# Kernel tuning notes

Measured on AMD Instinct MI355X. Metric: run time of the kernel, lower is better.

Reference implementation:

```python
import jax, jax.numpy as jnp
import numpy as np

EMB = 1024
HEADS = 16
HEAD_DIM = EMB // HEADS


def setup_inputs() -> dict:
    key = jax.random.key(0)
    ks = jax.random.split(key, 5)
    x = jax.random.normal(ks[0], (2, 2048, EMB), dtype=jnp.float32)
    # per-head projection params, stacked over heads: [H, E, D]
    Wq = jax.random.normal(ks[1], (HEADS, EMB, HEAD_DIM), dtype=jnp.float32)
    Wk = jax.random.normal(ks[2], (HEADS, EMB, HEAD_DIM), dtype=jnp.float32)
    Wv = jax.random.normal(ks[3], (HEADS, EMB, HEAD_DIM), dtype=jnp.float32)
    # output projection (torch Linear weight [out, in], bias=False)
    Wo = jax.random.normal(ks[4], (EMB, EMB), dtype=jnp.float32) * (1.0 / np.sqrt(EMB))
    return {"x": x, "Wq": Wq, "Wk": Wk, "Wv": Wv, "Wo": Wo}


def reference(x, Wq, Wk, Wv, Wo):
    B, T, E = x.shape
    # per-head projections: [B, H, T, D]
    q = jnp.einsum('bte,hed->bhtd', x, Wq)
    k = jnp.einsum('bte,hed->bhtd', x, Wk)
    v = jnp.einsum('bte,hed->bhtd', x, Wv)
    scale = 1.0 / jnp.sqrt(jnp.asarray(HEAD_DIM, dtype=x.dtype))
    scores = jnp.einsum('bhtd,bhsd->bhts', q, k) * scale  # [B,H,T,T]
    s = jax.nn.softmax(scores, axis=-1)
    out = jnp.einsum('bhts,bhsd->bhtd', s, v)
    # concat heads along last dim in head order: [B, T, H*D]
    combined = jnp.transpose(out, (0, 2, 1, 3)).reshape(B, T, E)
    # residual + output projection (Linear bias=False: y = combined @ Wo.T)
    return x + combined @ Wo.T
```

## Files before the change

### kernel.cpp

```cpp
#include <hip/hip_runtime.h>

#define EMB   1024
#define HEADS 16
#define HDIM  64
#define BATCH 2
#define SEQ   2048
#define MROWS (BATCH*SEQ)
#define STR   40
#define QSCALE 0.1803368801111204f

typedef __attribute__((ext_vector_type(8))) short bf16x8;
typedef __attribute__((ext_vector_type(4))) float f32x4;
typedef unsigned short u16;

__device__ __forceinline__ u16 f2bf(float f) {
    unsigned u = __float_as_uint(f);
    u += 0x7fffu + ((u >> 16) & 1u);
    return (u16)(u >> 16);
}
__device__ __forceinline__ float bf2f(u16 h) {
    return __uint_as_float((unsigned)h << 16);
}
__device__ __forceinline__ float fast_exp2(float x) {
#if __has_builtin(__builtin_amdgcn_exp2f)
    return __builtin_amdgcn_exp2f(x);
#else
    return __expf(x * 0.6931471805599453f);
#endif
}
__device__ __forceinline__ unsigned pk_trunc(float lo, float hi) {
    return __builtin_amdgcn_perm(__float_as_uint(hi), __float_as_uint(lo),
                                 0x07060302u);
}

#define SWZ(r, ch) ((((r) << 6)) + ((((ch) ^ ((r) & 7))) << 3))

__global__ __launch_bounds__(256)
void prep1(const float* __restrict__ X, const float* __restrict__ Wq,
           const float* __restrict__ Wk,
           u16* __restrict__ Xh, u16* __restrict__ Xl,
           u16* __restrict__ Qth, u16* __restrict__ Qtl,
           u16* __restrict__ Kth, u16* __restrict__ Ktl)
{
    const int bx = blockIdx.x;
    if (bx < 2048) {
        int i = (bx * 256 + threadIdx.x) * 8;
#pragma unroll
        for (int half = 0; half < 2; ++half) {
            float4 v = *(const float4*)(X + i + half * 4);
            ushort4 hi, lo;
            hi.x = f2bf(v.x); lo.x = f2bf(v.x - bf2f(hi.x));
            hi.y = f2bf(v.y); lo.y = f2bf(v.y - bf2f(hi.y));
            hi.z = f2bf(v.z); lo.z = f2bf(v.z - bf2f(hi.z));
            hi.w = f2bf(v.w); lo.w = f2bf(v.w - bf2f(hi.w));
            *(ushort4*)(Xh + i + half * 4) = hi;
            *(ushort4*)(Xl + i + half * 4) = lo;
        }
    } else {
        const int f = bx - 2048;
        const int z = f >> 9, y = (f >> 5) & 15, x = f & 31;
        const float* W  = z ? Wk  : Wq;
        u16* Oh         = z ? Kth : Qth;
        u16* Ol         = z ? Ktl : Qtl;
        const int d  = threadIdx.x & 63;
        const int e0 = (x * 4 + (threadIdx.x >> 6)) * 8;
        const float* src = W + ((size_t)y * EMB + e0) * HDIM + d;
        ushort4 h0, h1, l0, l1;
        float v; u16 hv;
        v = src[0 * 64]; hv = f2bf(v); h0.x = hv; l0.x = f2bf(v - bf2f(hv));
        v = src[1 * 64]; hv = f2bf(v); h0.y = hv; l0.y = f2bf(v - bf2f(hv));
        v = src[2 * 64]; hv = f2bf(v); h0.z = hv; l0.z = f2bf(v - bf2f(hv));
        v = src[3 * 64]; hv = f2bf(v); h0.w = hv; l0.w = f2bf(v - bf2f(hv));
        v = src[4 * 64]; hv = f2bf(v); h1.x = hv; l1.x = f2bf(v - bf2f(hv));
        v = src[5 * 64]; hv = f2bf(v); h1.y = hv; l1.y = f2bf(v - bf2f(hv));
        v = src[6 * 64]; hv = f2bf(v); h1.z = hv; l1.z = f2bf(v - bf2f(hv));
        v = src[7 * 64]; hv = f2bf(v); h1.w = hv; l1.w = f2bf(v - bf2f(hv));
        size_t obase = ((size_t)y * HDIM + d) * EMB + e0;
        *(ushort4*)(Oh + obase)     = h0;
        *(ushort4*)(Oh + obase + 4) = h1;
        *(ushort4*)(Ol + obase)     = l0;
        *(ushort4*)(Ol + obase + 4) = l1;
    }
}

__global__ __launch_bounds__(256)
void prep2(const float* __restrict__ Wv, const float* __restrict__ Wo,
           u16* __restrict__ Vth, u16* __restrict__ Woh)
{
    const int f = blockIdx.x;
    if (f < 512) {
        const int y = f >> 5, x = f & 31;
        const int d  = threadIdx.x & 63;
        const int e0 = (x * 4 + (threadIdx.x >> 6)) * 8;
        const float* src = Wv + ((size_t)y * EMB + e0) * HDIM + d;
        ushort4 h0, h1;
        h0.x = f2bf(src[0 * 64]); h0.y = f2bf(src[1 * 64]);
        h0.z = f2bf(src[2 * 64]); h0.w = f2bf(src[3 * 64]);
        h1.x = f2bf(src[4 * 64]); h1.y = f2bf(src[5 * 64]);
        h1.z = f2bf(src[6 * 64]); h1.w = f2bf(src[7 * 64]);
        size_t obase = ((size_t)y * HDIM + d) * EMB + e0;
        *(ushort4*)(Vth + obase)     = h0;
        *(ushort4*)(Vth + obase + 4) = h1;
    } else {
        int i = ((f - 512) * 256 + threadIdx.x) * 8;
#pragma unroll
        for (int half = 0; half < 2; ++half) {
            float4 v = *(const float4*)(Wo + i + half * 4);
            ushort4 o;
            o.x = f2bf(v.x); o.y = f2bf(v.y); o.z = f2bf(v.z); o.w = f2bf(v.w);
            *(ushort4*)(Woh + i + half * 4) = o;
        }
    }
}

__global__ __launch_bounds__(256, 2)
void qkv_z01(const u16* __restrict__ Xh, const u16* __restrict__ Xl,
             const u16* __restrict__ Wqh, const u16* __restrict__ Wql,
             const u16* __restrict__ Wkh, const u16* __restrict__ Wkl,
             u16* __restrict__ Qh, u16* __restrict__ Ql,
             u16* __restrict__ Kh, u16* __restrict__ Kl)
{
    const int z  = blockIdx.z;
    const int m0 = blockIdx.x * 128;
    const int n0 = blockIdx.y * 128;
    const int t    = threadIdx.x;
    const int wave = t >> 6, lane = t & 63;
    const int wm = wave & 1, wn = wave >> 1;
    const int l16 = lane & 15, quad = lane >> 4;

    __shared__ u16 Ahs[128][STR];
    __shared__ u16 Als[128][STR];
    __shared__ u16 Bhs[128][STR];
    __shared__ u16 Bls[128][STR];

    const u16* Bh_g = z ? Wkh : Wqh;
    const u16* Bl_g = z ? Wkl : Wql;

    const int ar0 = t >> 2, ak = (t & 3) * 8, ar1 = ar0 + 64;

    f32x4 acc[4][4];
#pragma unroll
    for (int i = 0; i < 4; ++i)
#pragma unroll
        for (int j = 0; j < 4; ++j) acc[i][j] = (f32x4){0.f, 0.f, 0.f, 0.f};

    bf16x8 cur[8], nxt[8], nx2[8];
#define QK_LOAD(dst, kk)                                                        \
    do {                                                                        \
        dst[0] = *(const bf16x8*)(Xh  + (size_t)(m0 + ar0) * EMB + (kk) + ak);  \
        dst[1] = *(const bf16x8*)(Xh  + (size_t)(m0 + ar1) * EMB + (kk) + ak);  \
        dst[2] = *(const bf16x8*)(Xl  + (size_t)(m0 + ar0) * EMB + (kk) + ak);  \
        dst[3] = *(const bf16x8*)(Xl  + (size_t)(m0 + ar1) * EMB + (kk) + ak);  \
        dst[4] = *(const bf16x8*)(Bh_g + (size_t)(n0 + ar0) * EMB + (kk) + ak); \
        dst[5] = *(const bf16x8*)(Bh_g + (size_t)(n0 + ar1) * EMB + (kk) + ak); \
        dst[6] = *(const bf16x8*)(Bl_g + (size_t)(n0 + ar0) * EMB + (kk) + ak); \
        dst[7] = *(const bf16x8*)(Bl_g + (size_t)(n0 + ar1) * EMB + (kk) + ak); \
    } while (0)

    QK_LOAD(cur, 0);
    QK_LOAD(nxt, 32);

    for (int k0 = 0; k0 < EMB; k0 += 32) {
        __syncthreads();
        *(bf16x8*)&Ahs[ar0][ak] = cur[0];  *(bf16x8*)&Ahs[ar1][ak] = cur[1];
        *(bf16x8*)&Als[ar0][ak] = cur[2];  *(bf16x8*)&Als[ar1][ak] = cur[3];
        *(bf16x8*)&Bhs[ar0][ak] = cur[4];  *(bf16x8*)&Bhs[ar1][ak] = cur[5];
        *(bf16x8*)&Bls[ar0][ak] = cur[6];  *(bf16x8*)&Bls[ar1][ak] = cur[7];
        __syncthreads();

        const int kn = (k0 + 64 < EMB) ? k0 + 64 : 0;
        QK_LOAD(nx2, kn);

        bf16x8 B4h[4], B4l[4];
#pragma unroll
        for (int j = 0; j < 4; ++j) {
            B4h[j] = *(const bf16x8*)&Bhs[wn * 64 + 16 * j + l16][quad * 8];
            B4l[j] = *(const bf16x8*)&Bls[wn * 64 + 16 * j + l16][quad * 8];
        }
#pragma unroll
        for (int i = 0; i < 4; ++i) {
            bf16x8 Ai_h = *(const bf16x8*)&Ahs[wm * 64 + 16 * i + l16][quad * 8];
            bf16x8 Ai_l = *(const bf16x8*)&Als[wm * 64 + 16 * i + l16][quad * 8];
#pragma unroll
            for (int j = 0; j < 4; ++j) {
                acc[i][j] = __builtin_amdgcn_mfma_f32_16x16x32_bf16(Ai_h, B4h[j], acc[i][j], 0, 0, 0);
                acc[i][j] = __builtin_amdgcn_mfma_f32_16x16x32_bf16(Ai_h, B4l[j], acc[i][j], 0, 0, 0);
                acc[i][j] = __builtin_amdgcn_mfma_f32_16x16x32_bf16(Ai_l, B4h[j], acc[i][j], 0, 0, 0);
            }
        }
#pragma unroll
        for (int q = 0; q < 8; ++q) { cur[q] = nxt[q]; nxt[q] = nx2[q]; }
    }
#undef QK_LOAD

    const int b = m0 >> 11;
    const int h = (n0 + wn * 64) >> 6;
    u16* Oh = z ? Kh : Qh;
    u16* Ol = z ? Kl : Ql;
    const float esc = z ? 1.0f : QSCALE;
#pragma unroll
    for (int i = 0; i < 4; ++i)
#pragma unroll
        for (int r = 0; r < 4; ++r) {
            int tt = (m0 & (SEQ - 1)) + wm * 64 + 16 * i + quad * 4 + r;
            size_t rowbase = ((size_t)(b * HEADS + h) * SEQ + tt) * HDIM;
#pragma unroll
            for (int j = 0; j < 4; ++j) {
                int d = 16 * j + l16;
                float v = acc[i][j][r] * esc;
                u16 hv = f2bf(v);
                Oh[rowbase + d] = hv;
                Ol[rowbase + d] = f2bf(v - bf2f(hv));
            }
        }
}

__global__ __launch_bounds__(256, 2)
void qkv_v(const u16* __restrict__ Xh, const u16* __restrict__ Wvt,
           u16* __restrict__ Vt)
{
    const int m0 = blockIdx.x * 128;
    const int n0 = blockIdx.y * 128;
    const int t    = threadIdx.x;
    const int wave = t >> 6, lane = t & 63;
    const int wm = wave & 1, wn = wave >> 1;
    const int l16 = lane & 15, quad = lane >> 4;

    __shared__ u16 Ahs[2][128][STR];
    __shared__ u16 Bhs[2][128][STR];

    const int ar0 = t >> 2, ak = (t & 3) * 8, ar1 = ar0 + 64;

    f32x4 acc[4][4];
#pragma unroll
    for (int i = 0; i < 4; ++i)
#pragma unroll
        for (int j = 0; j < 4; ++j) acc[i][j] = (f32x4){0.f, 0.f, 0.f, 0.f};

    bf16x8 cur[4];
#define V_LOAD(dst, kk)                                                         \
    do {                                                                        \
        dst[0] = *(const bf16x8*)(Xh  + (size_t)(m0 + ar0) * EMB + (kk) + ak);  \
        dst[1] = *(const bf16x8*)(Xh  + (size_t)(m0 + ar1) * EMB + (kk) + ak);  \
        dst[2] = *(const bf16x8*)(Wvt + (size_t)(n0 + ar0) * EMB + (kk) + ak);  \
        dst[3] = *(const bf16x8*)(Wvt + (size_t)(n0 + ar1) * EMB + (kk) + ak);  \
    } while (0)

    V_LOAD(cur, 0);
    *(bf16x8*)&Ahs[0][ar0][ak] = cur[0];  *(bf16x8*)&Ahs[0][ar1][ak] = cur[1];
    *(bf16x8*)&Bhs[0][ar0][ak] = cur[2];  *(bf16x8*)&Bhs[0][ar1][ak] = cur[3];

    for (int k0 = 0; k0 < EMB; k0 += 32) {
        const int buf = (k0 >> 5) & 1;
        __syncthreads();
        const int kn = (k0 + 32 < EMB) ? k0 + 32 : 0;
        V_LOAD(cur, kn);

        bf16x8 B4[4];
#pragma unroll
        for (int j = 0; j < 4; ++j)
            B4[j] = *(const bf16x8*)&Bhs[buf][wn * 64 + 16 * j + l16][quad * 8];
#pragma unroll
        for (int i = 0; i < 4; ++i) {
            bf16x8 Ai = *(const bf16x8*)&Ahs[buf][wm * 64 + 16 * i + l16][quad * 8];
#pragma unroll
            for (int j = 0; j < 4; ++j)
                acc[i][j] = __builtin_amdgcn_mfma_f32_16x16x32_bf16(Ai, B4[j], acc[i][j], 0, 0, 0);
        }
        *(bf16x8*)&Ahs[buf ^ 1][ar0][ak] = cur[0];
        *(bf16x8*)&Ahs[buf ^ 1][ar1][ak] = cur[1];
        *(bf16x8*)&Bhs[buf ^ 1][ar0][ak] = cur[2];
        *(bf16x8*)&Bhs[buf ^ 1][ar1][ak] = cur[3];
    }
#undef V_LOAD

    const int b = m0 >> 11;
    const int h = (n0 + wn * 64) >> 6;
#pragma unroll
    for (int i = 0; i < 4; ++i)
#pragma unroll
        for (int j = 0; j < 4; ++j) {
            int d  = 16 * j + l16;
            int tt = (m0 & (SEQ - 1)) + wm * 64 + 16 * i + quad * 4;
            ushort4 o;
            o.x = f2bf(acc[i][j][0]); o.y = f2bf(acc[i][j][1]);
            o.z = f2bf(acc[i][j][2]); o.w = f2bf(acc[i][j][3]);
            *(ushort4*)(Vt + ((size_t)(b * HEADS + h) * HDIM + d) * SEQ + tt) = o;
        }
}

__global__ __launch_bounds__(256, 2)
void attn_mfma(const u16* __restrict__ Qh, const u16* __restrict__ Ql,
               const u16* __restrict__ Kh, const u16* __restrict__ Kl,
               const u16* __restrict__ Vt, u16* __restrict__ Cb)
{
    const int qt0  = blockIdx.x * 128;
    const int bh   = blockIdx.y;
    const int t    = threadIdx.x;
    const int wave = t >> 6;
    const int lane = t & 63;
    const int l16  = lane & 15;
    const int quad = lane >> 4;

    __shared__ u16 Ksh[2][4096];
    __shared__ u16 Ksl[2][4096];
    __shared__ u16 Vs [2][4096];
    __shared__ u16 Ps [8192];

    const size_t bh_off = (size_t)bh * SEQ * HDIM;
    const u16* Qhb = Qh + bh_off;
    const u16* Qlb = Ql + bh_off;
    const u16* Khb = Kh + bh_off;
    const u16* Klb = Kl + bh_off;
    const u16* Vtb = Vt + bh_off;

    bf16x8 aQh[2][2], aQl[2][2];
#pragma unroll
    for (int g = 0; g < 2; ++g) {
        const int qrow = qt0 + g * 64 + wave * 16 + l16;
        const u16* bH = Qhb + (size_t)qrow * HDIM + quad * 8;
        const u16* bL = Qlb + (size_t)qrow * HDIM + quad * 8;
        aQh[g][0] = *(const bf16x8*)(bH);
        aQh[g][1] = *(const bf16x8*)(bH + 32);
        aQl[g][0] = *(const bf16x8*)(bL);
        aQl[g][1] = *(const bf16x8*)(bL + 32);
    }

    f32x4 accO[2][4];
    float m_i[2] = {-1e30f, -1e30f}, l_i[2] = {0.f, 0.f};
#pragma unroll
    for (int g = 0; g < 2; ++g)
#pragma unroll
        for (int j = 0; j < 4; ++j) accO[g][j] = (f32x4){0.f, 0.f, 0.f, 0.f};

    const int sr0 = t >> 3, sch = t & 7, sr1 = sr0 + 32;
    const int gc  = sch * 8;
    const int so0 = SWZ(sr0, sch), so1 = SWZ(sr1, sch);

    bf16x8 cur[6];
#define KV_LOAD(dst, ss)                                                       \
    do {                                                                       \
        dst[0] = *(const bf16x8*)(Khb + (size_t)((ss) + sr0) * HDIM + gc);     \
        dst[1] = *(const bf16x8*)(Khb + (size_t)((ss) + sr1) * HDIM + gc);     \
        dst[2] = *(const bf16x8*)(Klb + (size_t)((ss) + sr0) * HDIM + gc);     \
        dst[3] = *(const bf16x8*)(Klb + (size_t)((ss) + sr1) * HDIM + gc);     \
        dst[4] = *(const bf16x8*)(Vtb + (size_t)sr0 * SEQ + (ss) + gc);        \
        dst[5] = *(const bf16x8*)(Vtb + (size_t)sr1 * SEQ + (ss) + gc);        \
    } while (0)

    KV_LOAD(cur, 0);
    *(bf16x8*)&Ksh[0][so0] = cur[0];  *(bf16x8*)&Ksh[0][so1] = cur[1];
    *(bf16x8*)&Ksl[0][so0] = cur[2];  *(bf16x8*)&Ksl[0][so1] = cur[3];
    *(bf16x8*)&Vs [0][so0] = cur[4];  *(bf16x8*)&Vs [0][so1] = cur[5];

    for (int s0 = 0; s0 < SEQ; s0 += 64) {
        const int buf = (s0 >> 6) & 1;
        __syncthreads();
        const int sn = (s0 + 64 < SEQ) ? s0 + 64 : 0;
        KV_LOAD(cur, sn);

        f32x4 accS[2][4];
#pragma unroll
        for (int g = 0; g < 2; ++g)
#pragma unroll
            for (int i = 0; i < 4; ++i) accS[g][i] = (f32x4){0.f, 0.f, 0.f, 0.f};
#pragma unroll
        for (int c = 0; c < 2; ++c) {
#pragma unroll
            for (int i = 0; i < 4; ++i) {
                bf16x8 kh_ = *(const bf16x8*)&Ksh[buf][SWZ(16 * i + l16, 4 * c + quad)];
                bf16x8 kl_ = *(const bf16x8*)&Ksl[buf][SWZ(16 * i + l16, 4 * c + quad)];
                accS[0][i] = __builtin_amdgcn_mfma_f32_16x16x32_bf16(kh_, aQh[0][c], accS[0][i], 0, 0, 0);
                accS[0][i] = __builtin_amdgcn_mfma_f32_16x16x32_bf16(kl_, aQh[0][c], accS[0][i], 0, 0, 0);
                accS[0][i] = __builtin_amdgcn_mfma_f32_16x16x32_bf16(kh_, aQl[0][c], accS[0][i], 0, 0, 0);
                accS[1][i] = __builtin_amdgcn_mfma_f32_16x16x32_bf16(kh_, aQh[1][c], accS[1][i], 0, 0, 0);
                accS[1][i] = __builtin_amdgcn_mfma_f32_16x16x32_bf16(kl_, aQh[1][c], accS[1][i], 0, 0, 0);
                accS[1][i] = __builtin_amdgcn_mfma_f32_16x16x32_bf16(kh_, aQl[1][c], accS[1][i], 0, 0, 0);
            }
        }

#pragma unroll
        for (int g = 0; g < 2; ++g) {
            float vmax = fmaxf(fmaxf(accS[g][0][0], accS[g][0][1]),
                               fmaxf(accS[g][0][2], accS[g][0][3]));
#pragma unroll
            for (int i = 1; i < 4; ++i)
                vmax = fmaxf(vmax, fmaxf(fmaxf(accS[g][i][0], accS[g][i][1]),
                                         fmaxf(accS[g][i][2], accS[g][i][3])));
            vmax = fmaxf(vmax, __shfl_xor(vmax, 16, 64));
            vmax = fmaxf(vmax, __shfl_xor(vmax, 32, 64));
            float mn   = fmaxf(m_i[g], vmax);
            float alph = fast_exp2(m_i[g] - mn);
            m_i[g] = mn;
            float P[4][4], s = 0.f;
#pragma unroll
            for (int i = 0; i < 4; ++i)
#pragma unroll
                for (int r = 0; r < 4; ++r) {
                    P[i][r] = fast_exp2(accS[g][i][r] - mn);
                    s += P[i][r];
                }
            s += __shfl_xor(s, 16, 64);
            s += __shfl_xor(s, 32, 64);
            l_i[g] = l_i[g] * alph + s;
#pragma unroll
            for (int j = 0; j < 4; ++j) accO[g][j] *= alph;

            const int prow = g * 64 + wave * 16 + l16;
#pragma unroll
            for (int i = 0; i < 4; ++i) {
                uint2 pv;
                pv.x = pk_trunc(P[i][0], P[i][1]);
                pv.y = pk_trunc(P[i][2], P[i][3]);
                *(uint2*)&Ps[SWZ(prow, 2 * i + (quad >> 1)) + ((quad & 1) << 2)] = pv;
            }
        }

#pragma unroll
        for (int c = 0; c < 2; ++c) {
            bf16x8 bP0 = *(const bf16x8*)&Ps[SWZ(wave * 16 + l16,      4 * c + quad)];
            bf16x8 bP1 = *(const bf16x8*)&Ps[SWZ(64 + wave * 16 + l16, 4 * c + quad)];
#pragma unroll
            for (int j = 0; j < 4; ++j) {
                bf16x8 aV = *(const bf16x8*)&Vs[buf][SWZ(16 * j + l16, 4 * c + quad)];
                accO[0][j] = __builtin_amdgcn_mfma_f32_16x16x32_bf16(aV, bP0, accO[0][j], 0, 0, 0);
                accO[1][j] = __builtin_amdgcn_mfma_f32_16x16x32_bf16(aV, bP1, accO[1][j], 0, 0, 0);
            }
        }

        *(bf16x8*)&Ksh[buf ^ 1][so0] = cur[0];  *(bf16x8*)&Ksh[buf ^ 1][so1] = cur[1];
        *(bf16x8*)&Ksl[buf ^ 1][so0] = cur[2];  *(bf16x8*)&Ksl[buf ^ 1][so1] = cur[3];
        *(bf16x8*)&Vs [buf ^ 1][so0] = cur[4];  *(bf16x8*)&Vs [buf ^ 1][so1] = cur[5];
    }
#undef KV_LOAD

    const int b = bh >> 4, h = bh & 15;
#pragma unroll
    for (int g = 0; g < 2; ++g) {
        const int row = qt0 + g * 64 + wave * 16 + l16;
        const float inv = 1.f / l_i[g];
#pragma unroll
        for (int j = 0; j < 4; ++j) {
            ushort4 o;
            o.x = f2bf(accO[g][j][0] * inv); o.y = f2bf(accO[g][j][1] * inv);
            o.z = f2bf(accO[g][j][2] * inv); o.w = f2bf(accO[g][j][3] * inv);
            *(ushort4*)&Cb[((size_t)b * SEQ + row) * EMB + h * HDIM + 16 * j + quad * 4] = o;
        }
    }
}

__global__ __launch_bounds__(256, 2)
void oproj_mfma(const u16* __restrict__ Cb, const u16* __restrict__ Woh,
                const float* __restrict__ X, float* __restrict__ Y)
{
    const int m0 = blockIdx.x * 128;
    const int n0 = blockIdx.y * 128;
    const int t    = threadIdx.x;
    const int wave = t >> 6, lane = t & 63;
    const int wm = wave & 1, wn = wave >> 1;
    const int l16 = lane & 15, quad = lane >> 4;

    __shared__ u16 Ahs[2][128][STR];
    __shared__ u16 Bhs[2][128][STR];

    const int ar0 = t >> 2, ak = (t & 3) * 8, ar1 = ar0 + 64;

    f32x4 acc[4][4];
#pragma unroll
    for (int i = 0; i < 4; ++i)
#pragma unroll
        for (int j = 0; j < 4; ++j) acc[i][j] = (f32x4){0.f, 0.f, 0.f, 0.f};

    bf16x8 cur[4];
#define O_LOAD(dst, kk)                                                         \
    do {                                                                        \
        dst[0] = *(const bf16x8*)(Cb  + (size_t)(m0 + ar0) * EMB + (kk) + ak);  \
        dst[1] = *(const bf16x8*)(Cb  + (size_t)(m0 + ar1) * EMB + (kk) + ak);  \
        dst[2] = *(const bf16x8*)(Woh + (size_t)(n0 + ar0) * EMB + (kk) + ak);  \
        dst[3] = *(const bf16x8*)(Woh + (size_t)(n0 + ar1) * EMB + (kk) + ak);  \
    } while (0)

    O_LOAD(cur, 0);
    *(bf16x8*)&Ahs[0][ar0][ak] = cur[0];  *(bf16x8*)&Ahs[0][ar1][ak] = cur[1];
    *(bf16x8*)&Bhs[0][ar0][ak] = cur[2];  *(bf16x8*)&Bhs[0][ar1][ak] = cur[3];

    for (int k0 = 0; k0 < EMB; k0 += 32) {
        const int buf = (k0 >> 5) & 1;
        __syncthreads();
        const int kn = (k0 + 32 < EMB) ? k0 + 32 : 0;
        O_LOAD(cur, kn);

        bf16x8 B4[4];
#pragma unroll
        for (int j = 0; j < 4; ++j)
            B4[j] = *(const bf16x8*)&Bhs[buf][wn * 64 + 16 * j + l16][quad * 8];
#pragma unroll
        for (int i = 0; i < 4; ++i) {
            bf16x8 Ai = *(const bf16x8*)&Ahs[buf][wm * 64 + 16 * i + l16][quad * 8];
#pragma unroll
            for (int j = 0; j < 4; ++j)
                acc[i][j] = __builtin_amdgcn_mfma_f32_16x16x32_bf16(Ai, B4[j], acc[i][j], 0, 0, 0);
        }
        *(bf16x8*)&Ahs[buf ^ 1][ar0][ak] = cur[0];
        *(bf16x8*)&Ahs[buf ^ 1][ar1][ak] = cur[1];
        *(bf16x8*)&Bhs[buf ^ 1][ar0][ak] = cur[2];
        *(bf16x8*)&Bhs[buf ^ 1][ar1][ak] = cur[3];
    }
#undef O_LOAD

#pragma unroll
    for (int i = 0; i < 4; ++i)
#pragma unroll
        for (int r = 0; r < 4; ++r) {
            int m = m0 + wm * 64 + 16 * i + quad * 4 + r;
#pragma unroll
            for (int j = 0; j < 4; ++j) {
                int n = n0 + wn * 64 + 16 * j + l16;
                Y[(size_t)m * EMB + n] = acc[i][j][r] + X[(size_t)m * EMB + n];
            }
        }
}

extern "C" void kernel_launch(void* const* d_in, const int* in_sizes, int n_in,
                              void* d_out, int out_size, void* d_ws,
                              size_t ws_size, hipStream_t stream)
{
    const float* x  = (const float*)d_in[0];
    const float* Wq = (const float*)d_in[1];
    const float* Wk = (const float*)d_in[2];
    const float* Wv = (const float*)d_in[3];
    const float* Wo = (const float*)d_in[4];
    float* Y = (float*)d_out;

    const size_t NPER = (size_t)MROWS * EMB;
    u16* base  = (u16*)d_ws;
    u16* Qh    = base;
    u16* Ql    = Qh + NPER;
    u16* Kh    = Ql + NPER;
    u16* Kl    = Kh + NPER;
    u16* Vt    = Kl + NPER;
    u16* Xh    = Vt + NPER;
    u16* Xl    = Xh + NPER;
    u16* Wtq_h = Xl + NPER;
    u16* Wtq_l = Wtq_h + EMB * EMB;
    u16* Wtk_h = Wtq_l + EMB * EMB;
    u16* Wtk_l = Wtk_h + EMB * EMB;
    u16* Wvt   = Wtq_h;
    u16* Cb    = Xh;
    u16* Woh   = Xl;

    prep1<<<dim3(3072), 256, 0, stream>>>(x, Wq, Wk, Xh, Xl,
                                          Wtq_h, Wtq_l, Wtk_h, Wtk_l);
    qkv_z01<<<dim3(32, 8, 2), 256, 0, stream>>>(Xh, Xl, Wtq_h, Wtq_l,
                                                Wtk_h, Wtk_l, Qh, Ql, Kh, Kl);
    prep2<<<dim3(1024), 256, 0, stream>>>(Wv, Wo, Wvt, Woh);
    qkv_v<<<dim3(32, 8), 256, 0, stream>>>(Xh, Wvt, Vt);
    attn_mfma<<<dim3(SEQ / 128, BATCH * HEADS), 256, 0, stream>>>(Qh, Ql, Kh, Kl,
                                                                  Vt, Cb);
    oproj_mfma<<<dim3(32, 8), 256, 0, stream>>>(Cb, Woh, x, Y);
}
```

Baseline: 269.1 us.

## Double attention query tile per block and hoist K/V fragments into registers

Each attention block now handles 256 query rows (four 64-row groups) instead of 128, so every K/V tile read from global memory and LDS serves twice as many queries. K and V fragments are loaded from LDS into registers once per tile and reused across all groups. Scores are computed one group at a time to limit register pressure. The LDS double buffer becomes a single buffer with a register prefetch and an extra barrier per tile, and occupancy drops to one block per SIMD-set with half as many blocks (256), which may underfill the GPU.

```diff
diff --git a/kernel.cpp b/kernel.cpp
--- a/kernel.cpp
+++ b/kernel.cpp
@@ -289,12 +289,13 @@
         }
 }
 
-__global__ __launch_bounds__(256, 2)
+#define NG 4
+__global__ __launch_bounds__(256, 1)
 void attn_mfma(const u16* __restrict__ Qh, const u16* __restrict__ Ql,
                const u16* __restrict__ Kh, const u16* __restrict__ Kl,
                const u16* __restrict__ Vt, u16* __restrict__ Cb)
 {
-    const int qt0  = blockIdx.x * 128;
+    const int qt0  = blockIdx.x * 256;
     const int bh   = blockIdx.y;
     const int t    = threadIdx.x;
     const int wave = t >> 6;
@@ -302,10 +303,10 @@
     const int l16  = lane & 15;
     const int quad = lane >> 4;
 
-    __shared__ u16 Ksh[2][4096];
-    __shared__ u16 Ksl[2][4096];
-    __shared__ u16 Vs [2][4096];
-    __shared__ u16 Ps [8192];
+    __shared__ u16 Ksh[4096];
+    __shared__ u16 Ksl[4096];
+    __shared__ u16 Vs [4096];
+    __shared__ u16 Ps [16384];
 
     const size_t bh_off = (size_t)bh * SEQ * HDIM;
     const u16* Qhb = Qh + bh_off;
@@ -314,9 +315,9 @@
     const u16* Klb = Kl + bh_off;
     const u16* Vtb = Vt + bh_off;
 
-    bf16x8 aQh[2][2], aQl[2][2];
-#pragma unroll
-    for (int g = 0; g < 2; ++g) {
+    bf16x8 aQh[NG][2], aQl[NG][2];
+#pragma unroll
+    for (int g = 0; g < NG; ++g) {
         const int qrow = qt0 + g * 64 + wave * 16 + l16;
         const u16* bH = Qhb + (size_t)qrow * HDIM + quad * 8;
         const u16* bL = Qlb + (size_t)qrow * HDIM + quad * 8;
@@ -326,18 +327,20 @@
         aQl[g][1] = *(const bf16x8*)(bL + 32);
     }
 
-    f32x4 accO[2][4];
-    float m_i[2] = {-1e30f, -1e30f}, l_i[2] = {0.f, 0.f};
-#pragma unroll
-    for (int g = 0; g < 2; ++g)
+    f32x4 accO[NG][4];
+    float m_i[NG], l_i[NG];
+#pragma unroll
+    for (int g = 0; g < NG; ++g) {
+        m_i[g] = -1e30f; l_i[g] = 0.f;
 #pragma unroll
         for (int j = 0; j < 4; ++j) accO[g][j] = (f32x4){0.f, 0.f, 0.f, 0.f};
+    }
 
     const int sr0 = t >> 3, sch = t & 7, sr1 = sr0 + 32;
     const int gc  = sch * 8;
     const int so0 = SWZ(sr0, sch), so1 = SWZ(sr1, sch);
 
-    bf16x8 cur[6];
+    bf16x8 cur[6], nxt[6];
 #define KV_LOAD(dst, ss)                                                       \
     do {                                                                       \
         dst[0] = *(const bf16x8*)(Khb + (size_t)((ss) + sr0) * HDIM + gc);     \
@@ -349,44 +352,46 @@
     } while (0)
 
     KV_LOAD(cur, 0);
-    *(bf16x8*)&Ksh[0][so0] = cur[0];  *(bf16x8*)&Ksh[0][so1] = cur[1];
-    *(bf16x8*)&Ksl[0][so0] = cur[2];  *(bf16x8*)&Ksl[0][so1] = cur[3];
-    *(bf16x8*)&Vs [0][so0] = cur[4];  *(bf16x8*)&Vs [0][so1] = cur[5];
 
     for (int s0 = 0; s0 < SEQ; s0 += 64) {
-        const int buf = (s0 >> 6) & 1;
         __syncthreads();
+        *(bf16x8*)&Ksh[so0] = cur[0];  *(bf16x8*)&Ksh[so1] = cur[1];
+        *(bf16x8*)&Ksl[so0] = cur[2];  *(bf16x8*)&Ksl[so1] = cur[3];
+        *(bf16x8*)&Vs [so0] = cur[4];  *(bf16x8*)&Vs [so1] = cur[5];
+        __syncthreads();
+
         const int sn = (s0 + 64 < SEQ) ? s0 + 64 : 0;
-        KV_LOAD(cur, sn);
-
-        f32x4 accS[2][4];
-#pragma unroll
-        for (int g = 0; g < 2; ++g)
-#pragma unroll
-            for (int i = 0; i < 4; ++i) accS[g][i] = (f32x4){0.f, 0.f, 0.f, 0.f};
-#pragma unroll
-        for (int c = 0; c < 2; ++c) {
+        KV_LOAD(nxt, sn);
+
+        bf16x8 kh[2][4], kl[2][4];
+#pragma unroll
+        for (int c = 0; c < 2; ++c)
 #pragma unroll
             for (int i = 0; i < 4; ++i) {
-                bf16x8 kh_ = *(const bf16x8*)&Ksh[buf][SWZ(16 * i + l16, 4 * c + quad)];
-                bf16x8 kl_ = *(const bf16x8*)&Ksl[buf][SWZ(16 * i + l16, 4 * c + quad)];
-                accS[0][i] = __builtin_amdgcn_mfma_f32_16x16x32_bf16(kh_, aQh[0][c], accS[0][i], 0, 0, 0);
-                accS[0][i] = __builtin_amdgcn_mfma_f32_16x16x32_bf16(kl_, aQh[0][c], accS[0][i], 0, 0, 0);
-                accS[0][i] = __builtin_amdgcn_mfma_f32_16x16x32_bf16(kh_, aQl[0][c], accS[0][i], 0, 0, 0);
-                accS[1][i] = __builtin_amdgcn_mfma_f32_16x16x32_bf16(kh_, aQh[1][c], accS[1][i], 0, 0, 0);
-                accS[1][i] = __builtin_amdgcn_mfma_f32_16x16x32_bf16(kl_, aQh[1][c], accS[1][i], 0, 0, 0);
-                accS[1][i] = __builtin_amdgcn_mfma_f32_16x16x32_bf16(kh_, aQl[1][c], accS[1][i], 0, 0, 0);
+                kh[c][i] = *(const bf16x8*)&Ksh[SWZ(16 * i + l16, 4 * c + quad)];
+                kl[c][i] = *(const bf16x8*)&Ksl[SWZ(16 * i + l16, 4 * c + quad)];
             }
-        }
-
-#pragma unroll
-        for (int g = 0; g < 2; ++g) {
-            float vmax = fmaxf(fmaxf(accS[g][0][0], accS[g][0][1]),
-                               fmaxf(accS[g][0][2], accS[g][0][3]));
+
+#pragma unroll
+        for (int g = 0; g < NG; ++g) {
+            f32x4 accS[4];
+#pragma unroll
+            for (int i = 0; i < 4; ++i) accS[i] = (f32x4){0.f, 0.f, 0.f, 0.f};
+#pragma unroll
+            for (int c = 0; c < 2; ++c)
+#pragma unroll
+                for (int i = 0; i < 4; ++i) {
+                    accS[i] = __builtin_amdgcn_mfma_f32_16x16x32_bf16(kh[c][i], aQh[g][c], accS[i], 0, 0, 0);
+                    accS[i] = __builtin_amdgcn_mfma_f32_16x16x32_bf16(kl[c][i], aQh[g][c], accS[i], 0, 0, 0);
+                    accS[i] = __builtin_amdgcn_mfma_f32_16x16x32_bf16(kh[c][i], aQl[g][c], accS[i], 0, 0, 0);
+                }
+
+            float vmax = fmaxf(fmaxf(accS[0][0], accS[0][1]),
+                               fmaxf(accS[0][2], accS[0][3]));
 #pragma unroll
             for (int i = 1; i < 4; ++i)
-                vmax = fmaxf(vmax, fmaxf(fmaxf(accS[g][i][0], accS[g][i][1]),
-                                         fmaxf(accS[g][i][2], accS[g][i][3])));
+                vmax = fmaxf(vmax, fmaxf(fmaxf(accS[i][0], accS[i][1]),
+                                         fmaxf(accS[i][2], accS[i][3])));
             vmax = fmaxf(vmax, __shfl_xor(vmax, 16, 64));
             vmax = fmaxf(vmax, __shfl_xor(vmax, 32, 64));
             float mn   = fmaxf(m_i[g], vmax);
@@ -397,7 +402,7 @@
             for (int i = 0; i < 4; ++i)
 #pragma unroll
                 for (int r = 0; r < 4; ++r) {
-                    P[i][r] = fast_exp2(accS[g][i][r] - mn);
+                    P[i][r] = fast_exp2(accS[i][r] - mn);
                     s += P[i][r];
                 }
             s += __shfl_xor(s, 16, 64);
@@ -416,27 +421,29 @@
             }
         }
 
-#pragma unroll
-        for (int c = 0; c < 2; ++c) {
-            bf16x8 bP0 = *(const bf16x8*)&Ps[SWZ(wave * 16 + l16,      4 * c + quad)];
-            bf16x8 bP1 = *(const bf16x8*)&Ps[SWZ(64 + wave * 16 + l16, 4 * c + quad)];
-#pragma unroll
-            for (int j = 0; j < 4; ++j) {
-                bf16x8 aV = *(const bf16x8*)&Vs[buf][SWZ(16 * j + l16, 4 * c + quad)];
-                accO[0][j] = __builtin_amdgcn_mfma_f32_16x16x32_bf16(aV, bP0, accO[0][j], 0, 0, 0);
-                accO[1][j] = __builtin_amdgcn_mfma_f32_16x16x32_bf16(aV, bP1, accO[1][j], 0, 0, 0);
+        bf16x8 vv[2][4];
+#pragma unroll
+        for (int c = 0; c < 2; ++c)
+#pragma unroll
+            for (int j = 0; j < 4; ++j)
+                vv[c][j] = *(const bf16x8*)&Vs[SWZ(16 * j + l16, 4 * c + quad)];
+#pragma unroll
+        for (int g = 0; g < NG; ++g)
+#pragma unroll
+            for (int c = 0; c < 2; ++c) {
+                bf16x8 bP = *(const bf16x8*)&Ps[SWZ(g * 64 + wave * 16 + l16, 4 * c + quad)];
+#pragma unroll
+                for (int j = 0; j < 4; ++j)
+                    accO[g][j] = __builtin_amdgcn_mfma_f32_16x16x32_bf16(vv[c][j], bP, accO[g][j], 0, 0, 0);
             }
-        }
-
-        *(bf16x8*)&Ksh[buf ^ 1][so0] = cur[0];  *(bf16x8*)&Ksh[buf ^ 1][so1] = cur[1];
-        *(bf16x8*)&Ksl[buf ^ 1][so0] = cur[2];  *(bf16x8*)&Ksl[buf ^ 1][so1] = cur[3];
-        *(bf16x8*)&Vs [buf ^ 1][so0] = cur[4];  *(bf16x8*)&Vs [buf ^ 1][so1] = cur[5];
+#pragma unroll
+        for (int q = 0; q < 6; ++q) cur[q] = nxt[q];
     }
 #undef KV_LOAD
 
     const int b = bh >> 4, h = bh & 15;
 #pragma unroll
-    for (int g = 0; g < 2; ++g) {
+    for (int g = 0; g < NG; ++g) {
         const int row = qt0 + g * 64 + wave * 16 + l16;
         const float inv = 1.f / l_i[g];
 #pragma unroll
@@ -555,7 +562,7 @@
                                                 Wtk_h, Wtk_l, Qh, Ql, Kh, Kl);
     prep2<<<dim3(1024), 256, 0, stream>>>(Wv, Wo, Wvt, Woh);
     qkv_v<<<dim3(32, 8), 256, 0, stream>>>(Xh, Wvt, Vt);
-    attn_mfma<<<dim3(SEQ / 128, BATCH * HEADS), 256, 0, stream>>>(Qh, Ql, Kh, Kl,
+    attn_mfma<<<dim3(SEQ / 256, BATCH * HEADS), 256, 0, stream>>>(Qh, Ql, Kh, Kl,
                                                                   Vt, Cb);
     oproj_mfma<<<dim3(32, 8), 256, 0, stream>>>(Cb, Woh, x, Y);
 }
```

Measured after the change: 279.6 us. 3.9% more time.

## Split attention over key sequence halves and merge with a combine kernel

Applied to the files above, without the earlier changes.

The attention kernel now splits the key/value range into two halves along a third grid dimension. Each half writes a normalized partial output plus its row max and sum, and a new combine kernel merges the two with log-sum-exp weights. To allow four blocks per CU, LDS double buffering is replaced by a single buffer with register prefetch and an extra barrier per tile. Partial results and stats are staged in the output buffer before oproj overwrites it. This adds an extra kernel launch and memory traffic, and rounds each partial to bf16 before the merge.

```diff
diff --git a/kernel.cpp b/kernel.cpp
--- a/kernel.cpp
+++ b/kernel.cpp
@@ -8,6 +8,7 @@
 #define MROWS (BATCH*SEQ)
 #define STR   40
 #define QSCALE 0.1803368801111204f
+#define NRH   (BATCH*HEADS*SEQ)
 
 typedef __attribute__((ext_vector_type(8))) short bf16x8;
 typedef __attribute__((ext_vector_type(4))) float f32x4;
@@ -289,22 +290,26 @@
         }
 }
 
-__global__ __launch_bounds__(256, 2)
+__global__ __launch_bounds__(256, 4)
 void attn_mfma(const u16* __restrict__ Qh, const u16* __restrict__ Ql,
                const u16* __restrict__ Kh, const u16* __restrict__ Kl,
-               const u16* __restrict__ Vt, u16* __restrict__ Cb)
+               const u16* __restrict__ Vt, u16* __restrict__ P0,
+               u16* __restrict__ P1, float* __restrict__ ML)
 {
     const int qt0  = blockIdx.x * 128;
     const int bh   = blockIdx.y;
+    const int zs   = blockIdx.z;
+    const int sbeg = zs * (SEQ / 2);
+    const int send = sbeg + SEQ / 2;
     const int t    = threadIdx.x;
     const int wave = t >> 6;
     const int lane = t & 63;
     const int l16  = lane & 15;
     const int quad = lane >> 4;
 
-    __shared__ u16 Ksh[2][4096];
-    __shared__ u16 Ksl[2][4096];
-    __shared__ u16 Vs [2][4096];
+    __shared__ u16 Ksh[4096];
+    __shared__ u16 Ksl[4096];
+    __shared__ u16 Vs [4096];
     __shared__ u16 Ps [8192];
 
     const size_t bh_off = (size_t)bh * SEQ * HDIM;
@@ -337,7 +342,7 @@
     const int gc  = sch * 8;
     const int so0 = SWZ(sr0, sch), so1 = SWZ(sr1, sch);
 
-    bf16x8 cur[6];
+    bf16x8 cur[6], nxt[6];
 #define KV_LOAD(dst, ss)                                                       \
     do {                                                                       \
         dst[0] = *(const bf16x8*)(Khb + (size_t)((ss) + sr0) * HDIM + gc);     \
@@ -348,16 +353,17 @@
         dst[5] = *(const bf16x8*)(Vtb + (size_t)sr1 * SEQ + (ss) + gc);        \
     } while (0)
 
-    KV_LOAD(cur, 0);
-    *(bf16x8*)&Ksh[0][so0] = cur[0];  *(bf16x8*)&Ksh[0][so1] = cur[1];
-    *(bf16x8*)&Ksl[0][so0] = cur[2];  *(bf16x8*)&Ksl[0][so1] = cur[3];
-    *(bf16x8*)&Vs [0][so0] = cur[4];  *(bf16x8*)&Vs [0][so1] = cur[5];
-
-    for (int s0 = 0; s0 < SEQ; s0 += 64) {
-        const int buf = (s0 >> 6) & 1;
+    KV_LOAD(cur, sbeg);
+
+    for (int s0 = sbeg; s0 < send; s0 += 64) {
         __syncthreads();
-        const int sn = (s0 + 64 < SEQ) ? s0 + 64 : 0;
-        KV_LOAD(cur, sn);
+        *(bf16x8*)&Ksh[so0] = cur[0];  *(bf16x8*)&Ksh[so1] = cur[1];
+        *(bf16x8*)&Ksl[so0] = cur[2];  *(bf16x8*)&Ksl[so1] = cur[3];
+        *(bf16x8*)&Vs [so0] = cur[4];  *(bf16x8*)&Vs [so1] = cur[5];
+        __syncthreads();
+
+        const int sn = (s0 + 64 < send) ? s0 + 64 : sbeg;
+        KV_LOAD(nxt, sn);
 
         f32x4 accS[2][4];
 #pragma unroll
@@ -368,8 +374,8 @@
         for (int c = 0; c < 2; ++c) {
 #pragma unroll
             for (int i = 0; i < 4; ++i) {
-                bf16x8 kh_ = *(const bf16x8*)&Ksh[buf][SWZ(16 * i + l16, 4 * c + quad)];
-                bf16x8 kl_ = *(const bf16x8*)&Ksl[buf][SWZ(16 * i + l16, 4 * c + quad)];
+                bf16x8 kh_ = *(const bf16x8*)&Ksh[SWZ(16 * i + l16, 4 * c + quad)];
+                bf16x8 kl_ = *(const bf16x8*)&Ksl[SWZ(16 * i + l16, 4 * c + quad)];
                 accS[0][i] = __builtin_amdgcn_mfma_f32_16x16x32_bf16(kh_, aQh[0][c], accS[0][i], 0, 0, 0);
                 accS[0][i] = __builtin_amdgcn_mfma_f32_16x16x32_bf16(kl_, aQh[0][c], accS[0][i], 0, 0, 0);
                 accS[0][i] = __builtin_amdgcn_mfma_f32_16x16x32_bf16(kh_, aQl[0][c], accS[0][i], 0, 0, 0);
@@ -422,31 +428,64 @@
             bf16x8 bP1 = *(const bf16x8*)&Ps[SWZ(64 + wave * 16 + l16, 4 * c + quad)];
 #pragma unroll
             for (int j = 0; j < 4; ++j) {
-                bf16x8 aV = *(const bf16x8*)&Vs[buf][SWZ(16 * j + l16, 4 * c + quad)];
+                bf16x8 aV = *(const bf16x8*)&Vs[SWZ(16 * j + l16, 4 * c + quad)];
                 accO[0][j] = __builtin_amdgcn_mfma_f32_16x16x32_bf16(aV, bP0, accO[0][j], 0, 0, 0);
                 accO[1][j] = __builtin_amdgcn_mfma_f32_16x16x32_bf16(aV, bP1, accO[1][j], 0, 0, 0);
             }
         }
-
-        *(bf16x8*)&Ksh[buf ^ 1][so0] = cur[0];  *(bf16x8*)&Ksh[buf ^ 1][so1] = cur[1];
-        *(bf16x8*)&Ksl[buf ^ 1][so0] = cur[2];  *(bf16x8*)&Ksl[buf ^ 1][so1] = cur[3];
-        *(bf16x8*)&Vs [buf ^ 1][so0] = cur[4];  *(bf16x8*)&Vs [buf ^ 1][so1] = cur[5];
+#pragma unroll
+        for (int q = 0; q < 6; ++q) cur[q] = nxt[q];
     }
 #undef KV_LOAD
 
     const int b = bh >> 4, h = bh & 15;
+    u16*   Od = zs ? P1 : P0;
+    float* Mo = ML + (size_t)zs * (2 * NRH);
 #pragma unroll
     for (int g = 0; g < 2; ++g) {
         const int row = qt0 + g * 64 + wave * 16 + l16;
         const float inv = 1.f / l_i[g];
+        const size_t rh = (size_t)bh * SEQ + row;
+        Mo[rh]       = m_i[g];
+        Mo[NRH + rh] = l_i[g];
 #pragma unroll
         for (int j = 0; j < 4; ++j) {
             ushort4 o;
             o.x = f2bf(accO[g][j][0] * inv); o.y = f2bf(accO[g][j][1] * inv);
             o.z = f2bf(accO[g][j][2] * inv); o.w = f2bf(accO[g][j][3] * inv);
-            *(ushort4*)&Cb[((size_t)b * SEQ + row) * EMB + h * HDIM + 16 * j + quad * 4] = o;
-        }
-    }
+            *(ushort4*)&Od[((size_t)b * SEQ + row) * EMB + h * HDIM + 16 * j + quad * 4] = o;
+        }
+    }
+}
+
+__global__ __launch_bounds__(256)
+void attn_combine(u16* __restrict__ P0, const u16* __restrict__ P1,
+                  const float* __restrict__ ML)
+{
+    const int tid = blockIdx.x * 256 + threadIdx.x;
+    const int rh  = tid >> 4;
+    const int c4  = (tid & 15) * 4;
+    const int bh  = rh >> 11;
+    const int row = rh & (SEQ - 1);
+    const int b   = bh >> 4, h = bh & 15;
+
+    const float m0 = ML[rh],             l0 = ML[NRH + rh];
+    const float m1 = ML[2 * NRH + rh],   l1 = ML[3 * NRH + rh];
+    const float M  = fmaxf(m0, m1);
+    const float w0 = l0 * fast_exp2(m0 - M);
+    const float w1 = l1 * fast_exp2(m1 - M);
+    const float inv = 1.f / (w0 + w1);
+    const float a0 = w0 * inv, a1 = w1 * inv;
+
+    const size_t addr = ((size_t)b * SEQ + row) * EMB + h * HDIM + c4;
+    ushort4 o0 = *(const ushort4*)&P0[addr];
+    ushort4 o1 = *(const ushort4*)&P1[addr];
+    ushort4 o;
+    o.x = f2bf(bf2f(o0.x) * a0 + bf2f(o1.x) * a1);
+    o.y = f2bf(bf2f(o0.y) * a0 + bf2f(o1.y) * a1);
+    o.z = f2bf(bf2f(o0.z) * a0 + bf2f(o1.z) * a1);
+    o.w = f2bf(bf2f(o0.w) * a0 + bf2f(o1.w) * a1);
+    *(ushort4*)&P0[addr] = o;
 }
 
 __global__ __launch_bounds__(256, 2)
@@ -549,13 +588,17 @@
     u16* Cb    = Xh;
     u16* Woh   = Xl;
 
+    u16*   P1 = (u16*)d_out;
+    float* ML = (float*)((char*)d_out + 8u * 1024 * 1024);
+
     prep1<<<dim3(3072), 256, 0, stream>>>(x, Wq, Wk, Xh, Xl,
                                           Wtq_h, Wtq_l, Wtk_h, Wtk_l);
     qkv_z01<<<dim3(32, 8, 2), 256, 0, stream>>>(Xh, Xl, Wtq_h, Wtq_l,
                                                 Wtk_h, Wtk_l, Qh, Ql, Kh, Kl);
     prep2<<<dim3(1024), 256, 0, stream>>>(Wv, Wo, Wvt, Woh);
     qkv_v<<<dim3(32, 8), 256, 0, stream>>>(Xh, Wvt, Vt);
-    attn_mfma<<<dim3(SEQ / 128, BATCH * HEADS), 256, 0, stream>>>(Qh, Ql, Kh, Kl,
-                                                                  Vt, Cb);
+    attn_mfma<<<dim3(SEQ / 128, BATCH * HEADS, 2), 256, 0, stream>>>(
+        Qh, Ql, Kh, Kl, Vt, Cb, P1, ML);
+    attn_combine<<<dim3(4096), 256, 0, stream>>>(Cb, P1, ML);
     oproj_mfma<<<dim3(32, 8), 256, 0, stream>>>(Cb, Woh, x, Y);
 }
```

After: 336.9 us. 25.2% more time.

## Single-buffer attention LDS, raise occupancy, and remap blocks so each XCD shares heads

Applied to the files above, without the earlier changes.

Replaces the double-buffered K/V shared-memory tiles with a single buffer written at the top of each iteration between two barriers, while the next tile is prefetched into registers. This halves K/V LDS use and raises the launch-bounds target to four blocks per CU. The grid becomes 1D, and block indices are remapped so blocks on the same XCD (lin & 7) work on the same batch-head, for better L2 reuse of K/V. The cost is an extra barrier per iteration, less overlap of LDS writes with compute, and register pressure from holding both the cur and nxt register sets.

```diff
diff --git a/kernel.cpp b/kernel.cpp
--- a/kernel.cpp
+++ b/kernel.cpp
@@ -289,22 +289,25 @@
         }
 }
 
-__global__ __launch_bounds__(256, 2)
+__global__ __launch_bounds__(256, 4)
 void attn_mfma(const u16* __restrict__ Qh, const u16* __restrict__ Ql,
                const u16* __restrict__ Kh, const u16* __restrict__ Kl,
                const u16* __restrict__ Vt, u16* __restrict__ Cb)
 {
-    const int qt0  = blockIdx.x * 128;
-    const int bh   = blockIdx.y;
+    const int lin  = blockIdx.x;
+    const int xcd  = lin & 7;
+    const int slot = lin >> 3;
+    const int bh   = (slot >> 4) * 8 + xcd;
+    const int qt0  = (slot & 15) * 128;
     const int t    = threadIdx.x;
     const int wave = t >> 6;
     const int lane = t & 63;
     const int l16  = lane & 15;
     const int quad = lane >> 4;
 
-    __shared__ u16 Ksh[2][4096];
-    __shared__ u16 Ksl[2][4096];
-    __shared__ u16 Vs [2][4096];
+    __shared__ u16 Ksh[4096];
+    __shared__ u16 Ksl[4096];
+    __shared__ u16 Vs [4096];
     __shared__ u16 Ps [8192];
 
     const size_t bh_off = (size_t)bh * SEQ * HDIM;
@@ -337,7 +340,7 @@
     const int gc  = sch * 8;
     const int so0 = SWZ(sr0, sch), so1 = SWZ(sr1, sch);
 
-    bf16x8 cur[6];
+    bf16x8 cur[6], nxt[6];
 #define KV_LOAD(dst, ss)                                                       \
     do {                                                                       \
         dst[0] = *(const bf16x8*)(Khb + (size_t)((ss) + sr0) * HDIM + gc);     \
@@ -349,15 +352,16 @@
     } while (0)
 
     KV_LOAD(cur, 0);
-    *(bf16x8*)&Ksh[0][so0] = cur[0];  *(bf16x8*)&Ksh[0][so1] = cur[1];
-    *(bf16x8*)&Ksl[0][so0] = cur[2];  *(bf16x8*)&Ksl[0][so1] = cur[3];
-    *(bf16x8*)&Vs [0][so0] = cur[4];  *(bf16x8*)&Vs [0][so1] = cur[5];
 
     for (int s0 = 0; s0 < SEQ; s0 += 64) {
-        const int buf = (s0 >> 6) & 1;
         __syncthreads();
+        *(bf16x8*)&Ksh[so0] = cur[0];  *(bf16x8*)&Ksh[so1] = cur[1];
+        *(bf16x8*)&Ksl[so0] = cur[2];  *(bf16x8*)&Ksl[so1] = cur[3];
+        *(bf16x8*)&Vs [so0] = cur[4];  *(bf16x8*)&Vs [so1] = cur[5];
+        __syncthreads();
+
         const int sn = (s0 + 64 < SEQ) ? s0 + 64 : 0;
-        KV_LOAD(cur, sn);
+        KV_LOAD(nxt, sn);
 
         f32x4 accS[2][4];
 #pragma unroll
@@ -368,8 +372,8 @@
         for (int c = 0; c < 2; ++c) {
 #pragma unroll
             for (int i = 0; i < 4; ++i) {
-                bf16x8 kh_ = *(const bf16x8*)&Ksh[buf][SWZ(16 * i + l16, 4 * c + quad)];
-                bf16x8 kl_ = *(const bf16x8*)&Ksl[buf][SWZ(16 * i + l16, 4 * c + quad)];
+                bf16x8 kh_ = *(const bf16x8*)&Ksh[SWZ(16 * i + l16, 4 * c + quad)];
+                bf16x8 kl_ = *(const bf16x8*)&Ksl[SWZ(16 * i + l16, 4 * c + quad)];
                 accS[0][i] = __builtin_amdgcn_mfma_f32_16x16x32_bf16(kh_, aQh[0][c], accS[0][i], 0, 0, 0);
                 accS[0][i] = __builtin_amdgcn_mfma_f32_16x16x32_bf16(kl_, aQh[0][c], accS[0][i], 0, 0, 0);
                 accS[0][i] = __builtin_amdgcn_mfma_f32_16x16x32_bf16(kh_, aQl[0][c], accS[0][i], 0, 0, 0);
@@ -422,15 +426,13 @@
             bf16x8 bP1 = *(const bf16x8*)&Ps[SWZ(64 + wave * 16 + l16, 4 * c + quad)];
 #pragma unroll
             for (int j = 0; j < 4; ++j) {
-                bf16x8 aV = *(const bf16x8*)&Vs[buf][SWZ(16 * j + l16, 4 * c + quad)];
+                bf16x8 aV = *(const bf16x8*)&Vs[SWZ(16 * j + l16, 4 * c + quad)];
                 accO[0][j] = __builtin_amdgcn_mfma_f32_16x16x32_bf16(aV, bP0, accO[0][j], 0, 0, 0);
                 accO[1][j] = __builtin_amdgcn_mfma_f32_16x16x32_bf16(aV, bP1, accO[1][j], 0, 0, 0);
             }
         }
-
-        *(bf16x8*)&Ksh[buf ^ 1][so0] = cur[0];  *(bf16x8*)&Ksh[buf ^ 1][so1] = cur[1];
-        *(bf16x8*)&Ksl[buf ^ 1][so0] = cur[2];  *(bf16x8*)&Ksl[buf ^ 1][so1] = cur[3];
-        *(bf16x8*)&Vs [buf ^ 1][so0] = cur[4];  *(bf16x8*)&Vs [buf ^ 1][so1] = cur[5];
+#pragma unroll
+        for (int q = 0; q < 6; ++q) cur[q] = nxt[q];
     }
 #undef KV_LOAD
 
@@ -555,7 +557,6 @@
                                                 Wtk_h, Wtk_l, Qh, Ql, Kh, Kl);
     prep2<<<dim3(1024), 256, 0, stream>>>(Wv, Wo, Wvt, Woh);
     qkv_v<<<dim3(32, 8), 256, 0, stream>>>(Xh, Wvt, Vt);
-    attn_mfma<<<dim3(SEQ / 128, BATCH * HEADS), 256, 0, stream>>>(Qh, Ql, Kh, Kl,
-                                                                  Vt, Cb);
+    attn_mfma<<<dim3(512), 256, 0, stream>>>(Qh, Ql, Kh, Kl, Vt, Cb);
     oproj_mfma<<<dim3(32, 8), 256, 0, stream>>>(Cb, Woh, x, Y);
 }
```

Result: slower. 309.6 us (+15.0%).
